# Optimization experiments

Hardware: AMD Instinct MI355X
Metric: run time of the kernel (lower is better)

Reference implementation:

```python
import jax, jax.numpy as jnp
import numpy as np

SEQ, WORD, EMBED, NHEAD = 2048, 1024, 128, 16


def setup_inputs() -> dict:
    key = jax.random.key(0)
    ks = jax.random.split(key, 6)
    sw = 1.0 / np.sqrt(WORD)  # xavier-ish scale for linear weights
    sp = 1.0 / np.sqrt(EMBED * NHEAD)
    return {
        "x": jax.random.normal(ks[0], (SEQ, WORD), jnp.float32),
        "Wq": jax.random.normal(ks[1], (NHEAD, WORD, EMBED), jnp.float32) * sw,
        "bq": jnp.zeros((NHEAD, EMBED), jnp.float32),
        "Wk": jax.random.normal(ks[2], (NHEAD, WORD, EMBED), jnp.float32) * sw,
        "bk": jnp.zeros((NHEAD, EMBED), jnp.float32),
        "Wv": jax.random.normal(ks[3], (NHEAD, WORD, EMBED), jnp.float32) * sw,
        "bv": jnp.zeros((NHEAD, EMBED), jnp.float32),
        "proj": jax.random.normal(ks[4], (NHEAD * EMBED, EMBED), jnp.float32) * sp,
    }


def reference(x, Wq, bq, Wk, bk, Wv, bv, proj):
    # Batched-head equivalent of the per-head Attention ModuleList loop.
    # x: [S, W]; Wq/Wk/Wv: [H, W, E]; b*: [H, E]; proj: [H*E, E]
    Q = jnp.einsum("sw,hwe->hse", x, Wq) + bq[:, None, :]
    K = jnp.einsum("sw,hwe->hse", x, Wk) + bk[:, None, :]
    V = jnp.einsum("sw,hwe->hse", x, Wv) + bv[:, None, :]
    scale = 1.0 / jnp.sqrt(jnp.asarray(EMBED, x.dtype))
    scores = jnp.einsum("hqe,hke->hqk", Q, K) * scale  # [H, S, S]
    attn = jax.nn.softmax(scores, axis=-1)
    Z = jnp.einsum("hqk,hke->hqe", attn, V)  # [H, S, E]
    # torch.cat([...], dim=1): per-head outputs side-by-side -> [S, H*E]
    Z_s = jnp.transpose(Z, (1, 0, 2)).reshape(x.shape[0], -1)
    return Z_s @ proj  # [S, E]
```

## Files before the change

### kernel.cpp

```cpp
#include <hip/hip_runtime.h>
#include <stdint.h>

#define GAS __attribute__((address_space(1)))
#define LAS __attribute__((address_space(3)))

typedef unsigned short u16;
typedef __attribute__((ext_vector_type(8))) __bf16 bf16x8;
typedef __attribute__((ext_vector_type(4))) float f32x4;
typedef __attribute__((ext_vector_type(2))) unsigned int u32x2;
typedef __attribute__((ext_vector_type(4))) unsigned int u32x4;

#define SEQ 2048
#define WORD 1024
#define EMBED 128
#define NHEAD 16

__device__ __forceinline__ u16 f2b(float f) {
  return __builtin_bit_cast(u16, (__bf16)f);
}

__device__ __forceinline__ unsigned cvt_pk_bf16(float lo, float hi) {
  unsigned r;
  asm("v_cvt_pk_bf16_f32 %0, %1, %2" : "=v"(r) : "v"(lo), "v"(hi));
  return r;
}

__global__ __launch_bounds__(256) void cast_x_kernel(const float* __restrict__ x,
                                                     u16* __restrict__ xb) {
  int i = (blockIdx.x * 256 + threadIdx.x) * 4;
  float4 v = *(const float4*)(x + i);
  ushort4 o;
  o.x = f2b(v.x); o.y = f2b(v.y); o.z = f2b(v.z); o.w = f2b(v.w);
  *(ushort4*)(xb + i) = o;
}

__global__ __launch_bounds__(256) void transpose_cast_kernel(
    const float* __restrict__ s0, const float* __restrict__ s1,
    const float* __restrict__ s2, u16* __restrict__ d0, u16* __restrict__ d1,
    u16* __restrict__ d2, int R, int C, long stride, int zsel) {
  __shared__ float tile[32][33];
  const float* s;
  u16* d;
  if (zsel) {
    int z = blockIdx.z;
    int wsel = z >> 4, hh = z & 15;
    s = (wsel == 0 ? s0 : wsel == 1 ? s1 : s2) + (long)hh * stride;
    d = (wsel == 0 ? d0 : wsel == 1 ? d1 : d2) + (long)hh * stride;
  } else {
    s = s0; d = d0;
  }
  int r0 = blockIdx.x * 32, c0 = blockIdx.y * 32;
  int tx = threadIdx.x & 31, ty = threadIdx.x >> 5;
#pragma unroll
  for (int i = 0; i < 4; ++i)
    tile[ty + i * 8][tx] = s[(long)(r0 + ty + i * 8) * C + c0 + tx];
  __syncthreads();
#pragma unroll
  for (int i = 0; i < 4; ++i)
    d[(long)(c0 + ty + i * 8) * R + r0 + tx] = f2b(tile[tx][ty + i * 8]);
}

template <typename OUT>
__device__ __forceinline__ void gemm128(const u16* __restrict__ A, const u16* __restrict__ B,
                                        OUT* __restrict__ C, int lda, int ldb, int ldc,
                                        int ksteps, const float* biasN, const float* biasM,
                                        float scale) {
  __shared__ u16 lA[128 * 64];
  __shared__ u16 lB[128 * 64];
  const int tid = threadIdx.x;
  const int l = tid & 63, w = tid >> 6;
  const int quad = l >> 4, ln = l & 15;
  const int wm = w >> 1, wn = w & 1;
  f32x4 acc[4][4] = {};
  for (int ks = 0; ks < ksteps; ++ks) {
    const u16* Ak = A + ks * 64;
    const u16* Bk = B + ks * 64;
    __syncthreads();
#pragma unroll
    for (int i = 0; i < 4; ++i) {
      int idx = w * 256 + i * 64 + l;
      int r = idx >> 3, cp = idx & 7;
      int cg = cp ^ (r & 7);
      __builtin_amdgcn_global_load_lds((const GAS void*)(Ak + (long)r * lda + cg * 8),
                                       (LAS void*)(lA + (w * 256 + i * 64) * 8), 16, 0, 0);
      __builtin_amdgcn_global_load_lds((const GAS void*)(Bk + (long)r * ldb + cg * 8),
                                       (LAS void*)(lB + (w * 256 + i * 64) * 8), 16, 0, 0);
    }
    __syncthreads();
    bf16x8 af[2][4], bfv[2][4];
#pragma unroll
    for (int kc = 0; kc < 2; ++kc) {
#pragma unroll
      for (int i = 0; i < 4; ++i) {
        int c = kc * 4 + quad;
        int rm = wm * 64 + i * 16 + ln;
        af[kc][i] = *(const bf16x8*)(lA + rm * 64 + ((c ^ (rm & 7)) * 8));
        int rn = wn * 64 + i * 16 + ln;
        bfv[kc][i] = *(const bf16x8*)(lB + rn * 64 + ((c ^ (rn & 7)) * 8));
      }
    }
#pragma unroll
    for (int kc = 0; kc < 2; ++kc)
#pragma unroll
      for (int i = 0; i < 4; ++i)
#pragma unroll
        for (int j = 0; j < 4; ++j)
          acc[i][j] = __builtin_amdgcn_mfma_f32_16x16x32_bf16(af[kc][i], bfv[kc][j],
                                                              acc[i][j], 0, 0, 0);
  }
#pragma unroll
  for (int i = 0; i < 4; ++i) {
#pragma unroll
    for (int j = 0; j < 4; ++j) {
      int row0 = wm * 64 + i * 16 + quad * 4;
      int col = wn * 64 + j * 16 + ln;
      float bn = biasN ? biasN[col] : 0.f;
#pragma unroll
      for (int reg = 0; reg < 4; ++reg) {
        int row = row0 + reg;
        float bm = biasM ? biasM[row] : 0.f;
        float v = (acc[i][j][reg] + bn + bm) * scale;
        if constexpr (sizeof(OUT) == 2)
          C[(long)row * ldc + col] = (OUT)f2b(v);
        else
          C[(long)row * ldc + col] = v;
      }
    }
  }
}

__global__ __launch_bounds__(256, 3) void qkv_gemm_kernel(
    const u16* __restrict__ xb, const u16* __restrict__ Wqt, const u16* __restrict__ Wkt,
    const u16* __restrict__ Wvt, const float* __restrict__ bq, const float* __restrict__ bk,
    const float* __restrict__ bv, u16* __restrict__ Q, u16* __restrict__ Kb,
    u16* __restrict__ Vt) {
  const int t = blockIdx.x;
  const int h = blockIdx.y;
  const int which = blockIdx.z;
  const float qscale = 0.12753042123789493f;
  if (which == 0) {
    gemm128<u16>(xb + t * 128 * WORD, Wqt + h * EMBED * WORD,
                 Q + h * SEQ * EMBED + t * 128 * EMBED, WORD, WORD, EMBED,
                 WORD / 64, bq + h * EMBED, nullptr, qscale);
  } else if (which == 1) {
    gemm128<u16>(xb + t * 128 * WORD, Wkt + h * EMBED * WORD,
                 Kb + h * SEQ * EMBED + t * 128 * EMBED, WORD, WORD, EMBED,
                 WORD / 64, bk + h * EMBED, nullptr, 1.f);
  } else {
    gemm128<u16>(Wvt + h * EMBED * WORD, xb + t * 128 * WORD,
                 Vt + h * EMBED * SEQ + t * 128, WORD, WORD, SEQ,
                 WORD / 64, nullptr, bv + h * EMBED, 1.f);
  }
}

__global__ __launch_bounds__(512, 2) void attn_kernel(const u16* __restrict__ Q,
                                                      const u16* __restrict__ K,
                                                      const u16* __restrict__ V,
                                                      u16* __restrict__ Zs) {
  __shared__ __align__(16) u16 lKV[2][32768];
  const int bid = blockIdx.x;
  const int swz = (bid & 7) * 32 + (bid >> 3);
  const int h = swz >> 4, qb = swz & 15;
  const int tid = threadIdx.x;
  const int l = tid & 63, w = tid >> 6, quad = l >> 4, ln = l & 15;
  const int wr = w >> 1, wk = w & 1;
  const u16* Qh = Q + h * SEQ * EMBED;
  const u16* Kh = K + h * SEQ * EMBED;
  const u16* Vh = V + h * EMBED * SEQ;
  const int q0 = qb * 128 + wr * 32;

  auto stage = [&](int buf, int sup) {
#pragma unroll
    for (int j = 0; j < 4; ++j) {
      int kb = j >> 1;
      int cb = (j & 1) * 512 + w * 64;
      int c = cb + l;
      int rk = c >> 4, cgk = (c & 15) ^ (rk & 15);
      __builtin_amdgcn_global_load_lds(
          (const GAS void*)(Kh + (sup * 128 + kb * 64 + rk) * EMBED + cgk * 8),
          (LAS void*)(&lKV[buf][kb * 8192 + cb * 8]), 16, 0, 0);
      int rv = c >> 3, cgv = (c & 7) ^ (rv & 7);
      __builtin_amdgcn_global_load_lds(
          (const GAS void*)(Vh + rv * SEQ + sup * 128 + kb * 64 + cgv * 8),
          (LAS void*)(&lKV[buf][16384 + kb * 8192 + cb * 8]), 16, 0, 0);
    }
  };

  bf16x8 qf[2][4];
#pragma unroll
  for (int rs = 0; rs < 2; ++rs)
#pragma unroll
    for (int kc = 0; kc < 4; ++kc)
      qf[rs][kc] = *(const bf16x8*)(Qh + (q0 + rs * 16 + ln) * EMBED + kc * 32 + quad * 8);

  f32x4 oacc[2][8] = {};
  float rsum[2] = {0.f, 0.f};

  stage(0, 0);

  int cur = 0;
#pragma unroll 1
  for (int sup = 0; sup < SEQ / 128; ++sup) {
    if (sup + 1 < SEQ / 128) {
      stage(cur ^ 1, sup + 1);
      asm volatile("s_waitcnt vmcnt(8)" ::: "memory");
    } else {
      asm volatile("s_waitcnt vmcnt(0)" ::: "memory");
    }
    __builtin_amdgcn_s_barrier();
    __builtin_amdgcn_sched_barrier(0);

    const u16* myK = &lKV[cur][wk * 8192];
    const u16* myV = &lKV[cur][16384 + wk * 8192];

    f32x4 sacc[2][4] = {};
#pragma unroll
    for (int kc = 0; kc < 4; ++kc) {
      bf16x8 kf[4];
#pragma unroll
      for (int ns = 0; ns < 4; ++ns) {
        int kr = ns * 16 + ln;
        kf[ns] = *(const bf16x8*)(myK + kr * 128 + (((kc * 4 + quad) ^ (kr & 15)) * 8));
      }
      __builtin_amdgcn_s_setprio(1);
#pragma unroll
      for (int ns = 0; ns < 4; ++ns)
#pragma unroll
        for (int rs = 0; rs < 2; ++rs)
          sacc[rs][ns] = __builtin_amdgcn_mfma_f32_16x16x32_bf16(kf[ns], qf[rs][kc],
                                                                 sacc[rs][ns], 0, 0, 0);
      __builtin_amdgcn_s_setprio(0);
    }
    bf16x8 vf[2][8];
#pragma unroll
    for (int kc = 0; kc < 2; ++kc)
#pragma unroll
      for (int es = 0; es < 8; ++es) {
        int er = es * 16 + ln;
        vf[kc][es] = *(const bf16x8*)(myV + er * 64 + (((kc * 4 + quad) ^ (er & 7)) * 8));
      }
#pragma unroll
    for (int rs = 0; rs < 2; ++rs) {
      float p[4][4];
#pragma unroll
      for (int ns = 0; ns < 4; ++ns)
#pragma unroll
        for (int r = 0; r < 4; ++r) p[ns][r] = exp2f(sacc[rs][ns][r]);
      float s0 = (p[0][0] + p[0][1]) + (p[0][2] + p[0][3]);
      float s1 = (p[1][0] + p[1][1]) + (p[1][2] + p[1][3]);
      float s2 = (p[2][0] + p[2][1]) + (p[2][2] + p[2][3]);
      float s3 = (p[3][0] + p[3][1]) + (p[3][2] + p[3][3]);
      rsum[rs] += (s0 + s1) + (s2 + s3);
#pragma unroll
      for (int kc = 0; kc < 2; ++kc) {
        int n0 = kc * 2, n1 = kc * 2 + 1;
        unsigned a0 = cvt_pk_bf16(p[n0][0], p[n0][1]);
        unsigned a1 = cvt_pk_bf16(p[n0][2], p[n0][3]);
        unsigned b0 = cvt_pk_bf16(p[n1][0], p[n1][1]);
        unsigned b1 = cvt_pk_bf16(p[n1][2], p[n1][3]);
        u32x2 t0 = __builtin_amdgcn_permlane32_swap(a0, b0, false, false);
        u32x2 u0 = __builtin_amdgcn_permlane16_swap(t0.x, t0.y, false, false);
        u32x2 t1 = __builtin_amdgcn_permlane32_swap(a1, b1, false, false);
        u32x2 u1 = __builtin_amdgcn_permlane16_swap(t1.x, t1.y, false, false);
        u32x4 paw = {u0.x, u1.x, u0.y, u1.y};
        bf16x8 pa = __builtin_bit_cast(bf16x8, paw);
        __builtin_amdgcn_s_setprio(1);
#pragma unroll
        for (int es = 0; es < 8; ++es)
          oacc[rs][es] = __builtin_amdgcn_mfma_f32_16x16x32_bf16(pa, vf[kc][es],
                                                                 oacc[rs][es], 0, 0, 0);
        __builtin_amdgcn_s_setprio(0);
      }
    }
    __builtin_amdgcn_sched_barrier(0);
    __builtin_amdgcn_s_barrier();
    cur ^= 1;
  }

  float srl[2][4];
#pragma unroll
  for (int rs = 0; rs < 2; ++rs) {
    float t = rsum[rs] + __shfl(rsum[rs], l ^ 16);
    t = t + __shfl(t, l ^ 32);
#pragma unroll
    for (int r = 0; r < 4; ++r) srl[rs][r] = __shfl(t, quad * 4 + r);
  }

  __syncthreads();
  float* lO = (float*)lKV;
  if (wk == 1) {
#pragma unroll
    for (int rs = 0; rs < 2; ++rs) {
#pragma unroll
      for (int es = 0; es < 8; ++es)
#pragma unroll
        for (int r = 0; r < 4; ++r)
          lO[wr * 4224 + (rs * 16 + quad * 4 + r) * 132 + es * 16 + ln] = oacc[rs][es][r];
      if (ln == 0)
#pragma unroll
        for (int r = 0; r < 4; ++r)
          lO[wr * 4224 + (rs * 16 + quad * 4 + r) * 132 + 128] = srl[rs][r];
    }
  }
  __syncthreads();
  if (wk == 0) {
#pragma unroll
    for (int rs = 0; rs < 2; ++rs)
#pragma unroll
      for (int r = 0; r < 4; ++r) {
        int lrow = rs * 16 + quad * 4 + r;
        float lsum = srl[rs][r] + lO[wr * 4224 + lrow * 132 + 128];
        float rl = 1.f / lsum;
        int srow = q0 + lrow;
#pragma unroll
        for (int es = 0; es < 8; ++es) {
          float o = oacc[rs][es][r] + lO[wr * 4224 + lrow * 132 + es * 16 + ln];
          Zs[(long)srow * (NHEAD * EMBED) + h * EMBED + es * 16 + ln] = f2b(o * rl);
        }
      }
  }
}

__global__ __launch_bounds__(256, 2) void final_gemm_kernel(const u16* __restrict__ Zs,
                                                            const u16* __restrict__ projT,
                                                            float* __restrict__ pbuf) {
  const int t = blockIdx.x;
  const int kc = blockIdx.y;
  gemm128<float>(Zs + (long)t * 128 * (NHEAD * EMBED) + kc * 256, projT + kc * 256,
                 pbuf + (long)kc * SEQ * EMBED + t * 128 * EMBED,
                 NHEAD * EMBED, NHEAD * EMBED, EMBED, 4, nullptr, nullptr, 1.f);
}

__global__ __launch_bounds__(256) void reduce_kernel(const float* __restrict__ pbuf,
                                                     float* __restrict__ out) {
  int i = (blockIdx.x * 256 + threadIdx.x) * 4;
  float4 s = {0.f, 0.f, 0.f, 0.f};
#pragma unroll
  for (int kc = 0; kc < 8; ++kc) {
    float4 v = *(const float4*)(pbuf + (long)kc * SEQ * EMBED + i);
    s.x += v.x; s.y += v.y; s.z += v.z; s.w += v.w;
  }
  *(float4*)(out + i) = s;
}

extern "C" void kernel_launch(void* const* d_in, const int* in_sizes, int n_in,
                              void* d_out, int out_size, void* d_ws, size_t ws_size,
                              hipStream_t stream) {
  const float* x    = (const float*)d_in[0];
  const float* Wq   = (const float*)d_in[1];
  const float* bq   = (const float*)d_in[2];
  const float* Wk   = (const float*)d_in[3];
  const float* bk   = (const float*)d_in[4];
  const float* Wv   = (const float*)d_in[5];
  const float* bv   = (const float*)d_in[6];
  const float* proj = (const float*)d_in[7];
  float* out = (float*)d_out;

  char* ws = (char*)d_ws;
  u16* xb    = (u16*)(ws);
  u16* Wqt   = (u16*)(ws + (4L << 20));
  u16* Wkt   = (u16*)(ws + (8L << 20));
  u16* Wvt   = (u16*)(ws + (12L << 20));
  u16* projT = (u16*)(ws + (16L << 20));
  u16* Qm    = (u16*)(ws + (17L << 20));
  u16* Km    = (u16*)(ws + (26L << 20));
  u16* Vt    = (u16*)(ws + (35L << 20));
  u16* Zs    = (u16*)(ws + (44L << 20));
  float* pbuf = (float*)(ws);

  cast_x_kernel<<<dim3(SEQ * WORD / 1024), dim3(256), 0, stream>>>(x, xb);
  transpose_cast_kernel<<<dim3(WORD / 32, EMBED / 32, 48), dim3(256), 0, stream>>>(
      Wq, Wk, Wv, Wqt, Wkt, Wvt, WORD, EMBED, (long)WORD * EMBED, 1);
  transpose_cast_kernel<<<dim3(SEQ / 32, EMBED / 32, 1), dim3(256), 0, stream>>>(
      proj, nullptr, nullptr, projT, nullptr, nullptr, SEQ, EMBED, 0, 0);

  qkv_gemm_kernel<<<dim3(16, NHEAD, 3), dim3(256), 0, stream>>>(
      xb, Wqt, Wkt, Wvt, bq, bk, bv, Qm, Km, Vt);

  attn_kernel<<<dim3(256), dim3(512), 0, stream>>>(Qm, Km, Vt, Zs);

  final_gemm_kernel<<<dim3(16, 8), dim3(256), 0, stream>>>(Zs, projT, pbuf);
  reduce_kernel<<<dim3(SEQ * EMBED / 1024), dim3(256), 0, stream>>>(pbuf, out);
}
```

Before: 184.2 us.

## Halve attention tile sizes to double block count and occupancy

The attention kernel now processes 64 query rows per block (16 per wave) and streams K/V in 64-key chunks instead of 128, halving LDS use to 64 KB and doubling the grid to 512 blocks with launch bounds of 4 blocks per CU. The goal is to fill all CUs on the MI355X (256 blocks underfilled them) and raise occupancy for latency hiding. In exchange, each block reloads K/V for fewer query rows, which doubles global/L2 traffic for K/V. It also runs more loop iterations with barriers and has less MFMA work per LDS read.

Result: no change. 184.0 us (-0.1%).

```diff
diff --git a/kernel.cpp b/kernel.cpp
--- a/kernel.cpp
+++ b/kernel.cpp
@@ -153,171 +153,145 @@
   }
 }
 
-__global__ __launch_bounds__(512, 2) void attn_kernel(const u16* __restrict__ Q,
+__global__ __launch_bounds__(512, 4) void attn_kernel(const u16* __restrict__ Q,
                                                       const u16* __restrict__ K,
                                                       const u16* __restrict__ V,
                                                       u16* __restrict__ Zs) {
-  __shared__ __align__(16) u16 lKV[2][32768];
+  __shared__ __align__(16) u16 lKV[2][16384];
   const int bid = blockIdx.x;
-  const int swz = (bid & 7) * 32 + (bid >> 3);
-  const int h = swz >> 4, qb = swz & 15;
+  const int swz = (bid & 7) * 64 + (bid >> 3);
+  const int h = swz >> 5, qb = swz & 31;
   const int tid = threadIdx.x;
   const int l = tid & 63, w = tid >> 6, quad = l >> 4, ln = l & 15;
   const int wr = w >> 1, wk = w & 1;
   const u16* Qh = Q + h * SEQ * EMBED;
   const u16* Kh = K + h * SEQ * EMBED;
   const u16* Vh = V + h * EMBED * SEQ;
-  const int q0 = qb * 128 + wr * 32;
+  const int q0 = qb * 64 + wr * 16;
 
   auto stage = [&](int buf, int sup) {
 #pragma unroll
-    for (int j = 0; j < 4; ++j) {
-      int kb = j >> 1;
-      int cb = (j & 1) * 512 + w * 64;
-      int c = cb + l;
+    for (int j = 0; j < 2; ++j) {
+      int c = j * 512 + w * 64 + l;
       int rk = c >> 4, cgk = (c & 15) ^ (rk & 15);
       __builtin_amdgcn_global_load_lds(
-          (const GAS void*)(Kh + (sup * 128 + kb * 64 + rk) * EMBED + cgk * 8),
-          (LAS void*)(&lKV[buf][kb * 8192 + cb * 8]), 16, 0, 0);
+          (const GAS void*)(Kh + (sup * 64 + rk) * EMBED + cgk * 8),
+          (LAS void*)(&lKV[buf][c * 8]), 16, 0, 0);
       int rv = c >> 3, cgv = (c & 7) ^ (rv & 7);
       __builtin_amdgcn_global_load_lds(
-          (const GAS void*)(Vh + rv * SEQ + sup * 128 + kb * 64 + cgv * 8),
-          (LAS void*)(&lKV[buf][16384 + kb * 8192 + cb * 8]), 16, 0, 0);
+          (const GAS void*)(Vh + (long)rv * SEQ + sup * 64 + cgv * 8),
+          (LAS void*)(&lKV[buf][8192 + c * 8]), 16, 0, 0);
     }
   };
 
-  bf16x8 qf[2][4];
-#pragma unroll
-  for (int rs = 0; rs < 2; ++rs)
-#pragma unroll
-    for (int kc = 0; kc < 4; ++kc)
-      qf[rs][kc] = *(const bf16x8*)(Qh + (q0 + rs * 16 + ln) * EMBED + kc * 32 + quad * 8);
-
-  f32x4 oacc[2][8] = {};
-  float rsum[2] = {0.f, 0.f};
+  bf16x8 qf[4];
+#pragma unroll
+  for (int kc = 0; kc < 4; ++kc)
+    qf[kc] = *(const bf16x8*)(Qh + (q0 + ln) * EMBED + kc * 32 + quad * 8);
+
+  f32x4 oacc[8] = {};
+  float rsum = 0.f;
 
   stage(0, 0);
 
   int cur = 0;
 #pragma unroll 1
-  for (int sup = 0; sup < SEQ / 128; ++sup) {
-    if (sup + 1 < SEQ / 128) {
+  for (int sup = 0; sup < SEQ / 64; ++sup) {
+    if (sup + 1 < SEQ / 64) {
       stage(cur ^ 1, sup + 1);
-      asm volatile("s_waitcnt vmcnt(8)" ::: "memory");
+      asm volatile("s_waitcnt vmcnt(4)" ::: "memory");
     } else {
       asm volatile("s_waitcnt vmcnt(0)" ::: "memory");
     }
     __builtin_amdgcn_s_barrier();
     __builtin_amdgcn_sched_barrier(0);
 
-    const u16* myK = &lKV[cur][wk * 8192];
-    const u16* myV = &lKV[cur][16384 + wk * 8192];
-
-    f32x4 sacc[2][4] = {};
+    const u16* myK = &lKV[cur][0];
+    const u16* myV = &lKV[cur][8192];
+
+    f32x4 sacc[2] = {};
 #pragma unroll
     for (int kc = 0; kc < 4; ++kc) {
-      bf16x8 kf[4];
-#pragma unroll
-      for (int ns = 0; ns < 4; ++ns) {
-        int kr = ns * 16 + ln;
+      bf16x8 kf[2];
+#pragma unroll
+      for (int ns = 0; ns < 2; ++ns) {
+        int kr = wk * 32 + ns * 16 + ln;
         kf[ns] = *(const bf16x8*)(myK + kr * 128 + (((kc * 4 + quad) ^ (kr & 15)) * 8));
       }
       __builtin_amdgcn_s_setprio(1);
 #pragma unroll
-      for (int ns = 0; ns < 4; ++ns)
-#pragma unroll
-        for (int rs = 0; rs < 2; ++rs)
-          sacc[rs][ns] = __builtin_amdgcn_mfma_f32_16x16x32_bf16(kf[ns], qf[rs][kc],
-                                                                 sacc[rs][ns], 0, 0, 0);
+      for (int ns = 0; ns < 2; ++ns)
+        sacc[ns] = __builtin_amdgcn_mfma_f32_16x16x32_bf16(kf[ns], qf[kc], sacc[ns], 0, 0, 0);
       __builtin_amdgcn_s_setprio(0);
     }
-    bf16x8 vf[2][8];
-#pragma unroll
-    for (int kc = 0; kc < 2; ++kc)
-#pragma unroll
-      for (int es = 0; es < 8; ++es) {
-        int er = es * 16 + ln;
-        vf[kc][es] = *(const bf16x8*)(myV + er * 64 + (((kc * 4 + quad) ^ (er & 7)) * 8));
-      }
-#pragma unroll
-    for (int rs = 0; rs < 2; ++rs) {
-      float p[4][4];
-#pragma unroll
-      for (int ns = 0; ns < 4; ++ns)
-#pragma unroll
-        for (int r = 0; r < 4; ++r) p[ns][r] = exp2f(sacc[rs][ns][r]);
-      float s0 = (p[0][0] + p[0][1]) + (p[0][2] + p[0][3]);
-      float s1 = (p[1][0] + p[1][1]) + (p[1][2] + p[1][3]);
-      float s2 = (p[2][0] + p[2][1]) + (p[2][2] + p[2][3]);
-      float s3 = (p[3][0] + p[3][1]) + (p[3][2] + p[3][3]);
-      rsum[rs] += (s0 + s1) + (s2 + s3);
-#pragma unroll
-      for (int kc = 0; kc < 2; ++kc) {
-        int n0 = kc * 2, n1 = kc * 2 + 1;
-        unsigned a0 = cvt_pk_bf16(p[n0][0], p[n0][1]);
-        unsigned a1 = cvt_pk_bf16(p[n0][2], p[n0][3]);
-        unsigned b0 = cvt_pk_bf16(p[n1][0], p[n1][1]);
-        unsigned b1 = cvt_pk_bf16(p[n1][2], p[n1][3]);
-        u32x2 t0 = __builtin_amdgcn_permlane32_swap(a0, b0, false, false);
-        u32x2 u0 = __builtin_amdgcn_permlane16_swap(t0.x, t0.y, false, false);
-        u32x2 t1 = __builtin_amdgcn_permlane32_swap(a1, b1, false, false);
-        u32x2 u1 = __builtin_amdgcn_permlane16_swap(t1.x, t1.y, false, false);
-        u32x4 paw = {u0.x, u1.x, u0.y, u1.y};
-        bf16x8 pa = __builtin_bit_cast(bf16x8, paw);
-        __builtin_amdgcn_s_setprio(1);
-#pragma unroll
-        for (int es = 0; es < 8; ++es)
-          oacc[rs][es] = __builtin_amdgcn_mfma_f32_16x16x32_bf16(pa, vf[kc][es],
-                                                                 oacc[rs][es], 0, 0, 0);
-        __builtin_amdgcn_s_setprio(0);
-      }
+    bf16x8 vf[8];
+#pragma unroll
+    for (int es = 0; es < 8; ++es) {
+      int er = es * 16 + ln;
+      vf[es] = *(const bf16x8*)(myV + er * 64 + (((wk * 4 + quad) ^ (er & 7)) * 8));
+    }
+    float p[2][4];
+#pragma unroll
+    for (int ns = 0; ns < 2; ++ns)
+#pragma unroll
+      for (int r = 0; r < 4; ++r) p[ns][r] = exp2f(sacc[ns][r]);
+    rsum += ((p[0][0] + p[0][1]) + (p[0][2] + p[0][3])) +
+            ((p[1][0] + p[1][1]) + (p[1][2] + p[1][3]));
+    {
+      unsigned a0 = cvt_pk_bf16(p[0][0], p[0][1]);
+      unsigned a1 = cvt_pk_bf16(p[0][2], p[0][3]);
+      unsigned b0 = cvt_pk_bf16(p[1][0], p[1][1]);
+      unsigned b1 = cvt_pk_bf16(p[1][2], p[1][3]);
+      u32x2 t0 = __builtin_amdgcn_permlane32_swap(a0, b0, false, false);
+      u32x2 u0 = __builtin_amdgcn_permlane16_swap(t0.x, t0.y, false, false);
+      u32x2 t1 = __builtin_amdgcn_permlane32_swap(a1, b1, false, false);
+      u32x2 u1 = __builtin_amdgcn_permlane16_swap(t1.x, t1.y, false, false);
+      u32x4 paw = {u0.x, u1.x, u0.y, u1.y};
+      bf16x8 pa = __builtin_bit_cast(bf16x8, paw);
+      __builtin_amdgcn_s_setprio(1);
+#pragma unroll
+      for (int es = 0; es < 8; ++es)
+        oacc[es] = __builtin_amdgcn_mfma_f32_16x16x32_bf16(pa, vf[es], oacc[es], 0, 0, 0);
+      __builtin_amdgcn_s_setprio(0);
     }
     __builtin_amdgcn_sched_barrier(0);
     __builtin_amdgcn_s_barrier();
     cur ^= 1;
   }
 
-  float srl[2][4];
-#pragma unroll
-  for (int rs = 0; rs < 2; ++rs) {
-    float t = rsum[rs] + __shfl(rsum[rs], l ^ 16);
-    t = t + __shfl(t, l ^ 32);
-#pragma unroll
-    for (int r = 0; r < 4; ++r) srl[rs][r] = __shfl(t, quad * 4 + r);
-  }
+  float t = rsum + __shfl(rsum, l ^ 16);
+  t = t + __shfl(t, l ^ 32);
+  float srl[4];
+#pragma unroll
+  for (int r = 0; r < 4; ++r) srl[r] = __shfl(t, quad * 4 + r);
 
   __syncthreads();
   float* lO = (float*)lKV;
   if (wk == 1) {
 #pragma unroll
-    for (int rs = 0; rs < 2; ++rs) {
-#pragma unroll
-      for (int es = 0; es < 8; ++es)
-#pragma unroll
-        for (int r = 0; r < 4; ++r)
-          lO[wr * 4224 + (rs * 16 + quad * 4 + r) * 132 + es * 16 + ln] = oacc[rs][es][r];
-      if (ln == 0)
-#pragma unroll
-        for (int r = 0; r < 4; ++r)
-          lO[wr * 4224 + (rs * 16 + quad * 4 + r) * 132 + 128] = srl[rs][r];
-    }
+    for (int es = 0; es < 8; ++es)
+#pragma unroll
+      for (int r = 0; r < 4; ++r)
+        lO[wr * 2112 + (quad * 4 + r) * 132 + es * 16 + ln] = oacc[es][r];
+    if (ln == 0)
+#pragma unroll
+      for (int r = 0; r < 4; ++r)
+        lO[wr * 2112 + (quad * 4 + r) * 132 + 128] = srl[r];
   }
   __syncthreads();
   if (wk == 0) {
 #pragma unroll
-    for (int rs = 0; rs < 2; ++rs)
-#pragma unroll
-      for (int r = 0; r < 4; ++r) {
-        int lrow = rs * 16 + quad * 4 + r;
-        float lsum = srl[rs][r] + lO[wr * 4224 + lrow * 132 + 128];
-        float rl = 1.f / lsum;
-        int srow = q0 + lrow;
-#pragma unroll
-        for (int es = 0; es < 8; ++es) {
-          float o = oacc[rs][es][r] + lO[wr * 4224 + lrow * 132 + es * 16 + ln];
-          Zs[(long)srow * (NHEAD * EMBED) + h * EMBED + es * 16 + ln] = f2b(o * rl);
-        }
+    for (int r = 0; r < 4; ++r) {
+      int lrow = quad * 4 + r;
+      float lsum = srl[r] + lO[wr * 2112 + lrow * 132 + 128];
+      float rl = 1.f / lsum;
+      int srow = q0 + lrow;
+#pragma unroll
+      for (int es = 0; es < 8; ++es) {
+        float o = oacc[es][r] + lO[wr * 2112 + lrow * 132 + es * 16 + ln];
+        Zs[(long)srow * (NHEAD * EMBED) + h * EMBED + es * 16 + ln] = f2b(o * rl);
       }
+    }
   }
 }
 
@@ -377,7 +351,7 @@
   qkv_gemm_kernel<<<dim3(16, NHEAD, 3), dim3(256), 0, stream>>>(
       xb, Wqt, Wkt, Wvt, bq, bk, bv, Qm, Km, Vt);
 
-  attn_kernel<<<dim3(256), dim3(512), 0, stream>>>(Qm, Km, Vt, Zs);
+  attn_kernel<<<dim3(512), dim3(512), 0, stream>>>(Qm, Km, Vt, Zs);
 
   final_gemm_kernel<<<dim3(16, 8), dim3(256), 0, stream>>>(Zs, projT, pbuf);
   reduce_kernel<<<dim3(SEQ * EMBED / 1024), dim3(256), 0, stream>>>(pbuf, out);
```

## Merge preprocessing kernels into one launch and swizzle QKV GEMM block order

Applied to the files above, without the earlier changes.

Replaces three preprocessing launches (x cast, QKV weight transpose-cast, proj transpose-cast) with a single prep_kernel that dispatches on the block index. This removes two kernel launches and their gaps. It also remaps the QKV GEMM block index so that consecutive workgroups are spread in strides across (tile, head, which), which likely changes how work lands on the XCDs and improves L2 reuse of x and weight tiles. The cost is divergent block roles within one grid, and the remap only helps if it matches the hardware's dispatch pattern.

Result: faster. 173.7 us (median of 2 runs) (-5.7%).

```diff
diff --git a/kernel.cpp b/kernel.cpp
--- a/kernel.cpp
+++ b/kernel.cpp
@@ -25,39 +25,51 @@
   return r;
 }
 
-__global__ __launch_bounds__(256) void cast_x_kernel(const float* __restrict__ x,
-                                                     u16* __restrict__ xb) {
-  int i = (blockIdx.x * 256 + threadIdx.x) * 4;
-  float4 v = *(const float4*)(x + i);
-  ushort4 o;
-  o.x = f2b(v.x); o.y = f2b(v.y); o.z = f2b(v.z); o.w = f2b(v.w);
-  *(ushort4*)(xb + i) = o;
-}
-
-__global__ __launch_bounds__(256) void transpose_cast_kernel(
-    const float* __restrict__ s0, const float* __restrict__ s1,
-    const float* __restrict__ s2, u16* __restrict__ d0, u16* __restrict__ d1,
-    u16* __restrict__ d2, int R, int C, long stride, int zsel) {
+__global__ __launch_bounds__(256) void prep_kernel(
+    const float* __restrict__ x, const float* __restrict__ Wq,
+    const float* __restrict__ Wk, const float* __restrict__ Wv,
+    const float* __restrict__ proj, u16* __restrict__ xb, u16* __restrict__ Wqt,
+    u16* __restrict__ Wkt, u16* __restrict__ Wvt, u16* __restrict__ projT) {
   __shared__ float tile[32][33];
-  const float* s;
-  u16* d;
-  if (zsel) {
-    int z = blockIdx.z;
+  const int bid = blockIdx.x;
+  const int tid = threadIdx.x;
+  const int tx = tid & 31, ty = tid >> 5;
+  if (bid < 6144) {
+    int z = bid >> 7, xy = bid & 127;
+    int bx = xy & 31, by = xy >> 5;
     int wsel = z >> 4, hh = z & 15;
-    s = (wsel == 0 ? s0 : wsel == 1 ? s1 : s2) + (long)hh * stride;
-    d = (wsel == 0 ? d0 : wsel == 1 ? d1 : d2) + (long)hh * stride;
+    const float* s = (wsel == 0 ? Wq : wsel == 1 ? Wk : Wv) + (long)hh * (WORD * EMBED);
+    u16* d = (wsel == 0 ? Wqt : wsel == 1 ? Wkt : Wvt) + (long)hh * (WORD * EMBED);
+    int r0 = bx * 32, c0 = by * 32;
+#pragma unroll
+    for (int i = 0; i < 4; ++i)
+      tile[ty + i * 8][tx] = s[(long)(r0 + ty + i * 8) * EMBED + c0 + tx];
+    __syncthreads();
+#pragma unroll
+    for (int i = 0; i < 4; ++i)
+      d[(long)(c0 + ty + i * 8) * WORD + r0 + tx] = f2b(tile[tx][ty + i * 8]);
+  } else if (bid < 6400) {
+    int idx = bid - 6144;
+    int bx = idx & 63, by = idx >> 6;
+    int r0 = bx * 32, c0 = by * 32;
+#pragma unroll
+    for (int i = 0; i < 4; ++i)
+      tile[ty + i * 8][tx] = proj[(long)(r0 + ty + i * 8) * EMBED + c0 + tx];
+    __syncthreads();
+#pragma unroll
+    for (int i = 0; i < 4; ++i)
+      projT[(long)(c0 + ty + i * 8) * SEQ + r0 + tx] = f2b(tile[tx][ty + i * 8]);
   } else {
-    s = s0; d = d0;
-  }
-  int r0 = blockIdx.x * 32, c0 = blockIdx.y * 32;
-  int tx = threadIdx.x & 31, ty = threadIdx.x >> 5;
-#pragma unroll
-  for (int i = 0; i < 4; ++i)
-    tile[ty + i * 8][tx] = s[(long)(r0 + ty + i * 8) * C + c0 + tx];
-  __syncthreads();
-#pragma unroll
-  for (int i = 0; i < 4; ++i)
-    d[(long)(c0 + ty + i * 8) * R + r0 + tx] = f2b(tile[tx][ty + i * 8]);
+    long base = (long)(bid - 6400) * 4096;
+#pragma unroll
+    for (int k = 0; k < 4; ++k) {
+      long i = base + k * 1024 + tid * 4;
+      float4 v = *(const float4*)(x + i);
+      ushort4 o;
+      o.x = f2b(v.x); o.y = f2b(v.y); o.z = f2b(v.z); o.w = f2b(v.w);
+      *(ushort4*)(xb + i) = o;
+    }
+  }
 }
 
 template <typename OUT>
@@ -134,9 +146,11 @@
     const u16* __restrict__ Wvt, const float* __restrict__ bq, const float* __restrict__ bk,
     const float* __restrict__ bv, u16* __restrict__ Q, u16* __restrict__ Kb,
     u16* __restrict__ Vt) {
-  const int t = blockIdx.x;
-  const int h = blockIdx.y;
-  const int which = blockIdx.z;
+  const int lin = blockIdx.x + 16 * (blockIdx.y + 16 * blockIdx.z);
+  const int s = (lin & 7) * 96 + (lin >> 3);
+  const int t = s & 15;
+  const int h = (s >> 4) & 15;
+  const int which = s >> 8;
   const float qscale = 0.12753042123789493f;
   if (which == 0) {
     gemm128<u16>(xb + t * 128 * WORD, Wqt + h * EMBED * WORD,
@@ -368,11 +382,8 @@
   u16* Zs    = (u16*)(ws + (44L << 20));
   float* pbuf = (float*)(ws);
 
-  cast_x_kernel<<<dim3(SEQ * WORD / 1024), dim3(256), 0, stream>>>(x, xb);
-  transpose_cast_kernel<<<dim3(WORD / 32, EMBED / 32, 48), dim3(256), 0, stream>>>(
-      Wq, Wk, Wv, Wqt, Wkt, Wvt, WORD, EMBED, (long)WORD * EMBED, 1);
-  transpose_cast_kernel<<<dim3(SEQ / 32, EMBED / 32, 1), dim3(256), 0, stream>>>(
-      proj, nullptr, nullptr, projT, nullptr, nullptr, SEQ, EMBED, 0, 0);
+  prep_kernel<<<dim3(6912), dim3(256), 0, stream>>>(x, Wq, Wk, Wv, proj, xb, Wqt,
+                                                    Wkt, Wvt, projT);
 
   qkv_gemm_kernel<<<dim3(16, NHEAD, 3), dim3(256), 0, stream>>>(
       xb, Wqt, Wkt, Wvt, bq, bk, bv, Qm, Km, Vt);
```
